# Kernel tuning notes

Measured on AMD Instinct MI355X. Metric: run time of the kernel, lower is better.

The kernel has to match this reference:

```python
import jax, jax.numpy as jnp
import numpy as np

RANK = 16
LN_EPS = 1e-5


def _layer_norm(x, eps=LN_EPS):
    mu = jnp.mean(x, axis=-1, keepdims=True)
    var = jnp.var(x, axis=-1, keepdims=True)
    return (x - mu) / jnp.sqrt(var + eps)


def setup_inputs() -> dict:
    key = jax.random.key(0)
    ks = jax.random.split(key, 8)
    B, S, D, M, R = 32, 4096, 160, 16, RANK
    query = jax.random.normal(ks[0], (B, S, D), dtype=jnp.float32)
    interface = jax.random.normal(ks[1], (B, S, D), dtype=jnp.float32)
    memory = jax.random.normal(ks[2], (B, M, D), dtype=jnp.float32)
    sd = 1.0 / np.sqrt(D)
    sr = 1.0 / np.sqrt(R)
    # torch nn.Linear weights: [out_features, in_features]
    W_read_key = jax.random.uniform(ks[3], (R, D), minval=-sd, maxval=sd, dtype=jnp.float32)
    W_read_value = jax.random.uniform(ks[4], (D, R), minval=-sr, maxval=sr, dtype=jnp.float32)
    W_write_key = jax.random.uniform(ks[5], (R, D), minval=-sd, maxval=sd, dtype=jnp.float32)
    W_write_erase = jax.random.uniform(ks[6], (D, R), minval=-sr, maxval=sr, dtype=jnp.float32)
    W_write_add = jax.random.uniform(ks[7], (D, R), minval=-sr, maxval=sr, dtype=jnp.float32)
    return {
        "query": query,
        "interface": interface,
        "memory": memory,
        "W_read_key": W_read_key,
        "W_read_value": W_read_value,
        "W_write_key": W_write_key,
        "W_write_erase": W_write_erase,
        "W_write_add": W_write_add,
    }


def reference(query, interface, memory, W_read_key, W_read_value,
              W_write_key, W_write_erase, W_write_add):
    R = RANK
    # ---- read ----
    q_proj = jnp.einsum('bsd,rd->bsr', query, W_read_key)          # [B,S,R]
    mem_proj = memory[..., :R]                                      # [B,M,R]
    scores = jnp.einsum('bsr,bmr->bsm', q_proj, mem_proj) / jnp.sqrt(jnp.float32(R))
    attn = jax.nn.softmax(scores, axis=-1)                          # [B,S,M]
    content = jnp.einsum('bsm,bmd->bsd', attn, memory)              # [B,S,D]
    read_out = jnp.einsum('bsr,dr->bsd', content[..., :R], W_read_value)
    # ---- write ----
    i_mean = jnp.mean(interface, axis=1)                            # [B,D]
    i_proj = jnp.einsum('bd,rd->br', i_mean, W_write_key)           # [B,R]
    erase = jax.nn.sigmoid(jnp.einsum('br,dr->bd', i_proj, W_write_erase))[:, None, :]
    add = jnp.einsum('br,dr->bd', i_proj, W_write_add)[:, None, :]
    new_memory = _layer_norm(memory * (1.0 - erase) + add)          # [B,M,D]
    return read_out, new_memory
```

## Files before the change

kernel.cpp:

```cpp
#include <hip/hip_runtime.h>
#include <math.h>

#define NB 32
#define NS 4096
#define ND 160
#define ND4 40
#define NM 16
#define NR 16
#define TPB 64
#define NCB (NS / TPB)

__global__ __launch_bounds__(256, 5) void ulm_read_kernel(
    const float* __restrict__ query,
    const float* __restrict__ iface,
    const float* __restrict__ memory,
    const float* __restrict__ Wrk,
    const float* __restrict__ Wrv,
    float* __restrict__ read_out,
    float* __restrict__ ipart)
{
    __shared__ __align__(16) float sK[NM * ND];
    __shared__ __align__(16) float sV[NM * ND];
    __shared__ float sM16[NM * NR];
    __shared__ float4 sIred[4 * ND4];

    const int t = threadIdx.x;
    const int chunk = blockIdx.x;
    const int b = blockIdx.y;
    const int s0 = chunk * TPB;

    {
        int m = t >> 4, r = t & 15;
        sM16[t] = memory[((size_t)b * NM + m) * ND + r];
    }
    __syncthreads();

    if (t < ND) {
        float wk[NR], wv[NR];
#pragma unroll
        for (int r = 0; r < NR; ++r) wk[r] = Wrk[r * ND + t];
        const float4* wrv4 = reinterpret_cast<const float4*>(Wrv + t * NR);
#pragma unroll
        for (int j = 0; j < 4; ++j) {
            float4 v = wrv4[j];
            wv[j * 4 + 0] = v.x; wv[j * 4 + 1] = v.y;
            wv[j * 4 + 2] = v.z; wv[j * 4 + 3] = v.w;
        }
#pragma unroll
        for (int m = 0; m < NM; ++m) {
            float aK = 0.f, aV = 0.f;
#pragma unroll
            for (int r = 0; r < NR; ++r) {
                float mv = sM16[m * NR + r];
                aK += mv * wk[r];
                aV += mv * wv[r];
            }
            sK[m * ND + t] = aK * 0.25f;
            sV[m * ND + t] = aV;
        }
    }
    __syncthreads();

    const float4* sK4 = reinterpret_cast<const float4*>(sK);
    const float4* sV4 = reinterpret_cast<const float4*>(sV);

    const int l = t & 7;
    const int G = t >> 3;
    const int tok0 = G * 2, tok1 = tok0 + 1;

    const float4* q4 = reinterpret_cast<const float4*>(query + ((size_t)b * NS + s0) * ND);

    float sc0[NM], sc1[NM];
#pragma unroll
    for (int m = 0; m < NM; ++m) { sc0[m] = 0.f; sc1[m] = 0.f; }

#pragma unroll
    for (int k = 0; k < 5; ++k) {
        float4 qa = q4[tok0 * ND4 + l + 8 * k];
        float4 qb = q4[tok1 * ND4 + l + 8 * k];
#pragma unroll
        for (int m = 0; m < NM; ++m) {
            float4 kv = sK4[m * ND4 + l + 8 * k];
            sc0[m] += qa.x * kv.x + qa.y * kv.y + qa.z * kv.z + qa.w * kv.w;
            sc1[m] += qb.x * kv.x + qb.y * kv.y + qb.z * kv.z + qb.w * kv.w;
        }
    }
#pragma unroll
    for (int m = 0; m < NM; ++m) {
        sc0[m] += __shfl_xor(sc0[m], 1);
        sc0[m] += __shfl_xor(sc0[m], 2);
        sc0[m] += __shfl_xor(sc0[m], 4);
        sc1[m] += __shfl_xor(sc1[m], 1);
        sc1[m] += __shfl_xor(sc1[m], 2);
        sc1[m] += __shfl_xor(sc1[m], 4);
    }

    float mx0 = -1e30f, mx1 = -1e30f;
#pragma unroll
    for (int m = 0; m < NM; ++m) { mx0 = fmaxf(mx0, sc0[m]); mx1 = fmaxf(mx1, sc1[m]); }
    float sm0 = 0.f, sm1 = 0.f;
#pragma unroll
    for (int m = 0; m < NM; ++m) {
        sc0[m] = __expf(sc0[m] - mx0); sm0 += sc0[m];
        sc1[m] = __expf(sc1[m] - mx1); sm1 += sc1[m];
    }
    float inv0 = 1.f / sm0, inv1 = 1.f / sm1;
#pragma unroll
    for (int m = 0; m < NM; ++m) { sc0[m] *= inv0; sc1[m] *= inv1; }

    const float4* i4 = reinterpret_cast<const float4*>(iface + ((size_t)b * NS + s0) * ND);
    const int w = t >> 6;
#pragma unroll
    for (int k = 0; k < 5; ++k) {
        float4 va = i4[tok0 * ND4 + l + 8 * k];
        float4 vb = i4[tok1 * ND4 + l + 8 * k];
        float x = va.x + vb.x, y = va.y + vb.y;
        float z = va.z + vb.z, u = va.w + vb.w;
#pragma unroll
        for (int off = 8; off <= 32; off <<= 1) {
            x += __shfl_xor(x, off); y += __shfl_xor(y, off);
            z += __shfl_xor(z, off); u += __shfl_xor(u, off);
        }
        if ((t & 63) < 8) sIred[w * ND4 + k * 8 + l] = make_float4(x, y, z, u);
    }

    float4* out4 = reinterpret_cast<float4*>(read_out + ((size_t)b * NS + s0) * ND);
#pragma unroll
    for (int k = 0; k < 5; ++k) {
        float4 o0 = make_float4(0.f, 0.f, 0.f, 0.f);
        float4 o1 = make_float4(0.f, 0.f, 0.f, 0.f);
#pragma unroll
        for (int m = 0; m < NM; ++m) {
            float4 vv = sV4[m * ND4 + l + 8 * k];
            o0.x += sc0[m] * vv.x; o0.y += sc0[m] * vv.y;
            o0.z += sc0[m] * vv.z; o0.w += sc0[m] * vv.w;
            o1.x += sc1[m] * vv.x; o1.y += sc1[m] * vv.y;
            o1.z += sc1[m] * vv.z; o1.w += sc1[m] * vv.w;
        }
        out4[tok0 * ND4 + l + 8 * k] = o0;
        out4[tok1 * ND4 + l + 8 * k] = o1;
    }

    __syncthreads();
    if (t < ND4) {
        float4 a0 = sIred[t], a1 = sIred[ND4 + t];
        float4 a2 = sIred[2 * ND4 + t], a3 = sIred[3 * ND4 + t];
        float4 tot = make_float4(a0.x + a1.x + a2.x + a3.x,
                                 a0.y + a1.y + a2.y + a3.y,
                                 a0.z + a1.z + a2.z + a3.z,
                                 a0.w + a1.w + a2.w + a3.w);
        reinterpret_cast<float4*>(ipart + ((size_t)(b * NCB + chunk)) * ND)[t] = tot;
    }
}

__global__ __launch_bounds__(256) void ulm_write_kernel(
    const float* __restrict__ memory,
    const float* __restrict__ Wwk,
    const float* __restrict__ Wwe,
    const float* __restrict__ Wwa,
    const float* __restrict__ ipart,
    float* __restrict__ new_mem)
{
    __shared__ float sIm[ND];
    __shared__ float sIp[NR];
    __shared__ float sOmE[ND];
    __shared__ float sAdd[ND];

    const int b = blockIdx.x;
    const int t = threadIdx.x;

    if (t < ND) {
        float acc = 0.f;
        for (int c = 0; c < NCB; ++c)
            acc += ipart[((size_t)(b * NCB + c)) * ND + t];
        sIm[t] = acc * (1.0f / NS);
    }
    __syncthreads();

    if (t < NR) {
        float acc = 0.f;
        for (int d = 0; d < ND; ++d) acc += sIm[d] * Wwk[t * ND + d];
        sIp[t] = acc;
    }
    __syncthreads();

    if (t < ND) {
        float e = 0.f, a = 0.f;
#pragma unroll
        for (int r = 0; r < NR; ++r) {
            float ip = sIp[r];
            e += ip * Wwe[t * NR + r];
            a += ip * Wwa[t * NR + r];
        }
        sOmE[t] = 1.0f - 1.0f / (1.0f + __expf(-e));
        sAdd[t] = a;
    }
    __syncthreads();

    const int wave = t >> 6, lane = t & 63;
    for (int m = wave; m < NM; m += 4) {
        const float* mrow = memory + ((size_t)b * NM + m) * ND;
        float v0 = mrow[lane] * sOmE[lane] + sAdd[lane];
        float v1 = mrow[lane + 64] * sOmE[lane + 64] + sAdd[lane + 64];
        float v2 = 0.f;
        const bool has2 = lane < 32;
        if (has2) v2 = mrow[lane + 128] * sOmE[lane + 128] + sAdd[lane + 128];
        float s  = v0 + v1 + v2;
        float sq = v0 * v0 + v1 * v1 + v2 * v2;
#pragma unroll
        for (int off = 32; off; off >>= 1) {
            s  += __shfl_xor(s, off);
            sq += __shfl_xor(sq, off);
        }
        float mu   = s * (1.0f / ND);
        float var  = sq * (1.0f / ND) - mu * mu;
        float rstd = rsqrtf(var + 1e-5f);
        float* orow = new_mem + ((size_t)b * NM + m) * ND;
        orow[lane]      = (v0 - mu) * rstd;
        orow[lane + 64] = (v1 - mu) * rstd;
        if (has2) orow[lane + 128] = (v2 - mu) * rstd;
    }
}

extern "C" void kernel_launch(void* const* d_in, const int* in_sizes, int n_in,
                              void* d_out, int out_size, void* d_ws, size_t ws_size,
                              hipStream_t stream) {
    const float* query  = (const float*)d_in[0];
    const float* iface  = (const float*)d_in[1];
    const float* memory = (const float*)d_in[2];
    const float* Wrk    = (const float*)d_in[3];
    const float* Wrv    = (const float*)d_in[4];
    const float* Wwk    = (const float*)d_in[5];
    const float* Wwe    = (const float*)d_in[6];
    const float* Wwa    = (const float*)d_in[7];

    float* read_out = (float*)d_out;
    float* new_mem  = (float*)d_out + (size_t)NB * NS * ND;
    float* ipart    = (float*)d_ws;

    dim3 grid1(NCB, NB);
    ulm_read_kernel<<<grid1, 256, 0, stream>>>(query, iface, memory, Wrk, Wrv,
                                               read_out, ipart);
    ulm_write_kernel<<<NB, 256, 0, stream>>>(memory, Wwk, Wwe, Wwa, ipart, new_mem);
}
```

Baseline: 62.71 us.

## Precompute folded K/V per batch in separate kernel and stream output stores

Moves the per-batch fold of memory with the read weights out of every read block into a small pre-kernel that writes the K/V tables to workspace. Read blocks then load K/V straight from global memory (L1/L2-cached) instead of recomputing them into shared memory, and the occupancy hint rises from 5 to 6. Outputs are written with nontemporal stores, and the partial-sum loop in the write kernel is unrolled. The cost is an extra kernel launch, and the inner loops now read K/V from global memory rather than LDS.

```diff
diff --git a/kernel.cpp b/kernel.cpp
--- a/kernel.cpp
+++ b/kernel.cpp
@@ -10,31 +10,22 @@
 #define TPB 64
 #define NCB (NS / TPB)
 
-__global__ __launch_bounds__(256, 5) void ulm_read_kernel(
-    const float* __restrict__ query,
-    const float* __restrict__ iface,
+typedef float f32x4 __attribute__((ext_vector_type(4)));
+
+__global__ __launch_bounds__(256) void ulm_fold_kv(
     const float* __restrict__ memory,
     const float* __restrict__ Wrk,
     const float* __restrict__ Wrv,
-    float* __restrict__ read_out,
-    float* __restrict__ ipart)
+    float* __restrict__ kvbuf)
 {
-    __shared__ __align__(16) float sK[NM * ND];
-    __shared__ __align__(16) float sV[NM * ND];
     __shared__ float sM16[NM * NR];
-    __shared__ float4 sIred[4 * ND4];
-
+    const int b = blockIdx.x;
     const int t = threadIdx.x;
-    const int chunk = blockIdx.x;
-    const int b = blockIdx.y;
-    const int s0 = chunk * TPB;
-
     {
         int m = t >> 4, r = t & 15;
         sM16[t] = memory[((size_t)b * NM + m) * ND + r];
     }
     __syncthreads();
-
     if (t < ND) {
         float wk[NR], wv[NR];
 #pragma unroll
@@ -46,6 +37,7 @@
             wv[j * 4 + 0] = v.x; wv[j * 4 + 1] = v.y;
             wv[j * 4 + 2] = v.z; wv[j * 4 + 3] = v.w;
         }
+        float* kb = kvbuf + (size_t)b * 2 * NM * ND;
 #pragma unroll
         for (int m = 0; m < NM; ++m) {
             float aK = 0.f, aV = 0.f;
@@ -55,14 +47,28 @@
                 aK += mv * wk[r];
                 aV += mv * wv[r];
             }
-            sK[m * ND + t] = aK * 0.25f;
-            sV[m * ND + t] = aV;
-        }
-    }
-    __syncthreads();
-
-    const float4* sK4 = reinterpret_cast<const float4*>(sK);
-    const float4* sV4 = reinterpret_cast<const float4*>(sV);
+            kb[m * ND + t]           = aK * 0.25f;
+            kb[NM * ND + m * ND + t] = aV;
+        }
+    }
+}
+
+__global__ __launch_bounds__(256, 6) void ulm_read_kernel(
+    const float* __restrict__ query,
+    const float* __restrict__ iface,
+    const float* __restrict__ kvbuf,
+    float* __restrict__ read_out,
+    float* __restrict__ ipart)
+{
+    __shared__ float4 sIred[4 * ND4];
+
+    const int t = threadIdx.x;
+    const int chunk = blockIdx.x;
+    const int b = blockIdx.y;
+    const int s0 = chunk * TPB;
+
+    const float4* kK4 = reinterpret_cast<const float4*>(kvbuf + (size_t)b * 2 * NM * ND);
+    const float4* kV4 = kK4 + NM * ND4;
 
     const int l = t & 7;
     const int G = t >> 3;
@@ -80,7 +86,7 @@
         float4 qb = q4[tok1 * ND4 + l + 8 * k];
 #pragma unroll
         for (int m = 0; m < NM; ++m) {
-            float4 kv = sK4[m * ND4 + l + 8 * k];
+            float4 kv = kK4[m * ND4 + l + 8 * k];
             sc0[m] += qa.x * kv.x + qa.y * kv.y + qa.z * kv.z + qa.w * kv.w;
             sc1[m] += qb.x * kv.x + qb.y * kv.y + qb.z * kv.z + qb.w * kv.w;
         }
@@ -131,14 +137,18 @@
         float4 o1 = make_float4(0.f, 0.f, 0.f, 0.f);
 #pragma unroll
         for (int m = 0; m < NM; ++m) {
-            float4 vv = sV4[m * ND4 + l + 8 * k];
+            float4 vv = kV4[m * ND4 + l + 8 * k];
             o0.x += sc0[m] * vv.x; o0.y += sc0[m] * vv.y;
             o0.z += sc0[m] * vv.z; o0.w += sc0[m] * vv.w;
             o1.x += sc1[m] * vv.x; o1.y += sc1[m] * vv.y;
             o1.z += sc1[m] * vv.z; o1.w += sc1[m] * vv.w;
         }
-        out4[tok0 * ND4 + l + 8 * k] = o0;
-        out4[tok1 * ND4 + l + 8 * k] = o1;
+        f32x4 ov0; ov0.x = o0.x; ov0.y = o0.y; ov0.z = o0.z; ov0.w = o0.w;
+        f32x4 ov1; ov1.x = o1.x; ov1.y = o1.y; ov1.z = o1.z; ov1.w = o1.w;
+        __builtin_nontemporal_store(ov0,
+            reinterpret_cast<f32x4*>(out4 + tok0 * ND4 + l + 8 * k));
+        __builtin_nontemporal_store(ov1,
+            reinterpret_cast<f32x4*>(out4 + tok1 * ND4 + l + 8 * k));
     }
 
     __syncthreads();
@@ -171,6 +181,7 @@
 
     if (t < ND) {
         float acc = 0.f;
+#pragma unroll 8
         for (int c = 0; c < NCB; ++c)
             acc += ipart[((size_t)(b * NCB + c)) * ND + t];
         sIm[t] = acc * (1.0f / NS);
@@ -237,9 +248,11 @@
     float* read_out = (float*)d_out;
     float* new_mem  = (float*)d_out + (size_t)NB * NS * ND;
     float* ipart    = (float*)d_ws;
-
+    float* kvbuf    = (float*)d_ws + (size_t)NB * NCB * ND;
+
+    ulm_fold_kv<<<NB, 256, 0, stream>>>(memory, Wrk, Wrv, kvbuf);
     dim3 grid1(NCB, NB);
-    ulm_read_kernel<<<grid1, 256, 0, stream>>>(query, iface, memory, Wrk, Wrv,
+    ulm_read_kernel<<<grid1, 256, 0, stream>>>(query, iface, kvbuf,
                                                read_out, ipart);
     ulm_write_kernel<<<NB, 256, 0, stream>>>(memory, Wwk, Wwe, Wwa, ipart, new_mem);
 }
```

New measurement: 176.1 us. +180.9%, slower.

## Compute attention scores and value projection with bf16 MFMA

Applied to the files above, without the earlier changes.

Rewrites the read kernel so the query-key score product and the attention-value product run on 16x16x32 bf16 MFMA instructions, with operands rounded from fp32 to bf16. Each block now covers 256 tokens, processed by each wave in sets of 16, and the softmax probabilities pass through shared memory to be repacked as MFMA fragments. The interface sum becomes a per-lane accumulation over 8 tokens. This cuts the scalar FMA work of the fp32 kernel, at the cost of bf16 precision in the scores and outputs and fewer blocks in the grid.

```diff
diff --git a/kernel.cpp b/kernel.cpp
--- a/kernel.cpp
+++ b/kernel.cpp
@@ -1,4 +1,5 @@
 #include <hip/hip_runtime.h>
+#include <hip/hip_bf16.h>
 #include <math.h>
 
 #define NB 32
@@ -7,10 +8,29 @@
 #define ND4 40
 #define NM 16
 #define NR 16
-#define TPB 64
+#define TPB 256
 #define NCB (NS / TPB)
 
-__global__ __launch_bounds__(256, 5) void ulm_read_kernel(
+typedef float  f32x4  __attribute__((ext_vector_type(4)));
+typedef short  bf16x8 __attribute__((ext_vector_type(8)));
+typedef unsigned int u32x4 __attribute__((ext_vector_type(4)));
+
+__device__ __forceinline__ unsigned bfpair(float lo, float hi) {
+    union { float f; unsigned u; } a, c;
+    a.f = lo; c.f = hi;
+    unsigned ua = (a.u + 0x7FFFu + ((a.u >> 16) & 1u)) >> 16;
+    unsigned uc = (c.u + 0x7FFFu + ((c.u >> 16) & 1u)) >> 16;
+    return (uc << 16) | (ua & 0xFFFFu);
+}
+
+__device__ __forceinline__ bf16x8 mkfrag(unsigned w0, unsigned w1,
+                                         unsigned w2, unsigned w3) {
+    union { u32x4 u; bf16x8 h; } x;
+    x.u = (u32x4){w0, w1, w2, w3};
+    return x.h;
+}
+
+__global__ __launch_bounds__(256) void ulm_read_kernel(
     const float* __restrict__ query,
     const float* __restrict__ iface,
     const float* __restrict__ memory,
@@ -19,20 +39,21 @@
     float* __restrict__ read_out,
     float* __restrict__ ipart)
 {
-    __shared__ __align__(16) float sK[NM * ND];
-    __shared__ __align__(16) float sV[NM * ND];
+    __shared__ __align__(16) float sKV[2 * NM * ND];
     __shared__ float sM16[NM * NR];
+    __shared__ unsigned sP[4][16 * 10];
     __shared__ float4 sIred[4 * ND4];
 
     const int t = threadIdx.x;
     const int chunk = blockIdx.x;
     const int b = blockIdx.y;
     const int s0 = chunk * TPB;
-
-    {
-        int m = t >> 4, r = t & 15;
-        sM16[t] = memory[((size_t)b * NM + m) * ND + r];
-    }
+    const int w  = t >> 6;
+    const int l  = t & 63;
+    const int lr = l & 15;
+    const int lg = l >> 4;
+
+    sM16[t] = memory[((size_t)b * NM + (t >> 4)) * ND + (t & 15)];
     __syncthreads();
 
     if (t < ND) {
@@ -55,92 +76,118 @@
                 aK += mv * wk[r];
                 aV += mv * wv[r];
             }
-            sK[m * ND + t] = aK * 0.25f;
-            sV[m * ND + t] = aV;
-        }
-    }
-    __syncthreads();
-
-    const float4* sK4 = reinterpret_cast<const float4*>(sK);
-    const float4* sV4 = reinterpret_cast<const float4*>(sV);
-
-    const int l = t & 7;
-    const int G = t >> 3;
-    const int tok0 = G * 2, tok1 = tok0 + 1;
-
-    const float4* q4 = reinterpret_cast<const float4*>(query + ((size_t)b * NS + s0) * ND);
-
-    float sc0[NM], sc1[NM];
-#pragma unroll
-    for (int m = 0; m < NM; ++m) { sc0[m] = 0.f; sc1[m] = 0.f; }
-
+            sKV[m * ND + t]           = aK * 0.25f;
+            sKV[NM * ND + m * ND + t] = aV;
+        }
+    }
+    __syncthreads();
+
+    bf16x8 kf[5];
+#pragma unroll
+    for (int kb = 0; kb < 5; ++kb) {
+        const float* src = &sKV[lr * ND + lg * 8 + kb * 32];
+        float4 a = *reinterpret_cast<const float4*>(src);
+        float4 c = *reinterpret_cast<const float4*>(src + 4);
+        kf[kb] = mkfrag(bfpair(a.x, a.y), bfpair(a.z, a.w),
+                        bfpair(c.x, c.y), bfpair(c.z, c.w));
+    }
+
+    bf16x8 vf[10];
+#pragma unroll
+    for (int d = 0; d < 10; ++d) {
+        if (lg < 2) {
+            float f0 = sKV[NM*ND + (lg*8 + 0) * ND + d*16 + lr];
+            float f1 = sKV[NM*ND + (lg*8 + 1) * ND + d*16 + lr];
+            float f2 = sKV[NM*ND + (lg*8 + 2) * ND + d*16 + lr];
+            float f3 = sKV[NM*ND + (lg*8 + 3) * ND + d*16 + lr];
+            float f4 = sKV[NM*ND + (lg*8 + 4) * ND + d*16 + lr];
+            float f5 = sKV[NM*ND + (lg*8 + 5) * ND + d*16 + lr];
+            float f6 = sKV[NM*ND + (lg*8 + 6) * ND + d*16 + lr];
+            float f7 = sKV[NM*ND + (lg*8 + 7) * ND + d*16 + lr];
+            vf[d] = mkfrag(bfpair(f0, f1), bfpair(f2, f3),
+                           bfpair(f4, f5), bfpair(f6, f7));
+        } else {
+            vf[d] = mkfrag(0u, 0u, 0u, 0u);
+        }
+    }
+
+    const size_t base = (size_t)b * NS * ND;
+    const float4* q4  = reinterpret_cast<const float4*>(query + base) + (size_t)s0 * ND4;
+    float4* out4      = reinterpret_cast<float4*>(read_out + base) + (size_t)s0 * ND4;
+    const int wtok0 = w * 64;
+    unsigned* pl = &sP[w][0];
+
+#pragma unroll 1
+    for (int set = 0; set < 4; ++set) {
+        const int tok = wtok0 + set * 16 + lr;
+
+        float4 qr[10];
+#pragma unroll
+        for (int kb = 0; kb < 5; ++kb) {
+            qr[2*kb]   = q4[(size_t)tok * ND4 + lg * 2 + kb * 8];
+            qr[2*kb+1] = q4[(size_t)tok * ND4 + lg * 2 + kb * 8 + 1];
+        }
+
+        f32x4 D = {0.f, 0.f, 0.f, 0.f};
+#pragma unroll
+        for (int kb = 0; kb < 5; ++kb) {
+            bf16x8 qf = mkfrag(bfpair(qr[2*kb].x,   qr[2*kb].y),
+                               bfpair(qr[2*kb].z,   qr[2*kb].w),
+                               bfpair(qr[2*kb+1].x, qr[2*kb+1].y),
+                               bfpair(qr[2*kb+1].z, qr[2*kb+1].w));
+            D = __builtin_amdgcn_mfma_f32_16x16x32_bf16(kf[kb], qf, D, 0, 0, 0);
+        }
+
+        float mx = fmaxf(fmaxf(D[0], D[1]), fmaxf(D[2], D[3]));
+        mx = fmaxf(mx, __shfl_xor(mx, 16));
+        mx = fmaxf(mx, __shfl_xor(mx, 32));
+        float e0 = __expf(D[0] - mx), e1 = __expf(D[1] - mx);
+        float e2 = __expf(D[2] - mx), e3 = __expf(D[3] - mx);
+        float sm = e0 + e1 + e2 + e3;
+        sm += __shfl_xor(sm, 16);
+        sm += __shfl_xor(sm, 32);
+        float inv = 1.f / sm;
+        e0 *= inv; e1 *= inv; e2 *= inv; e3 *= inv;
+
+        pl[lr * 10 + lg * 2 + 0] = bfpair(e0, e1);
+        pl[lr * 10 + lg * 2 + 1] = bfpair(e2, e3);
+        asm volatile("s_waitcnt lgkmcnt(0)" ::: "memory");
+        int pb = (lg < 2) ? (lr * 10 + lg * 4) : 0;
+        bf16x8 pf = mkfrag(pl[pb], pl[pb + 1], pl[pb + 2], pl[pb + 3]);
+
+#pragma unroll
+        for (int d = 0; d < 10; ++d) {
+            f32x4 D2 = {0.f, 0.f, 0.f, 0.f};
+            D2 = __builtin_amdgcn_mfma_f32_16x16x32_bf16(vf[d], pf, D2, 0, 0, 0);
+            out4[(size_t)tok * ND4 + d * 4 + lg] =
+                make_float4(D2[0], D2[1], D2[2], D2[3]);
+        }
+    }
+
+    const float4* i4 = reinterpret_cast<const float4*>(iface + base) + (size_t)s0 * ND4;
+    const int l8 = l & 7, g8 = l >> 3;
+    float4 ia[5];
+#pragma unroll
+    for (int k = 0; k < 5; ++k) ia[k] = make_float4(0.f, 0.f, 0.f, 0.f);
+#pragma unroll
+    for (int i = 0; i < 8; ++i) {
+        int tk = wtok0 + g8 * 8 + i;
+#pragma unroll
+        for (int k = 0; k < 5; ++k) {
+            float4 v = i4[(size_t)tk * ND4 + l8 + 8 * k];
+            ia[k].x += v.x; ia[k].y += v.y; ia[k].z += v.z; ia[k].w += v.w;
+        }
+    }
 #pragma unroll
     for (int k = 0; k < 5; ++k) {
-        float4 qa = q4[tok0 * ND4 + l + 8 * k];
-        float4 qb = q4[tok1 * ND4 + l + 8 * k];
-#pragma unroll
-        for (int m = 0; m < NM; ++m) {
-            float4 kv = sK4[m * ND4 + l + 8 * k];
-            sc0[m] += qa.x * kv.x + qa.y * kv.y + qa.z * kv.z + qa.w * kv.w;
-            sc1[m] += qb.x * kv.x + qb.y * kv.y + qb.z * kv.z + qb.w * kv.w;
-        }
-    }
-#pragma unroll
-    for (int m = 0; m < NM; ++m) {
-        sc0[m] += __shfl_xor(sc0[m], 1);
-        sc0[m] += __shfl_xor(sc0[m], 2);
-        sc0[m] += __shfl_xor(sc0[m], 4);
-        sc1[m] += __shfl_xor(sc1[m], 1);
-        sc1[m] += __shfl_xor(sc1[m], 2);
-        sc1[m] += __shfl_xor(sc1[m], 4);
-    }
-
-    float mx0 = -1e30f, mx1 = -1e30f;
-#pragma unroll
-    for (int m = 0; m < NM; ++m) { mx0 = fmaxf(mx0, sc0[m]); mx1 = fmaxf(mx1, sc1[m]); }
-    float sm0 = 0.f, sm1 = 0.f;
-#pragma unroll
-    for (int m = 0; m < NM; ++m) {
-        sc0[m] = __expf(sc0[m] - mx0); sm0 += sc0[m];
-        sc1[m] = __expf(sc1[m] - mx1); sm1 += sc1[m];
-    }
-    float inv0 = 1.f / sm0, inv1 = 1.f / sm1;
-#pragma unroll
-    for (int m = 0; m < NM; ++m) { sc0[m] *= inv0; sc1[m] *= inv1; }
-
-    const float4* i4 = reinterpret_cast<const float4*>(iface + ((size_t)b * NS + s0) * ND);
-    const int w = t >> 6;
-#pragma unroll
-    for (int k = 0; k < 5; ++k) {
-        float4 va = i4[tok0 * ND4 + l + 8 * k];
-        float4 vb = i4[tok1 * ND4 + l + 8 * k];
-        float x = va.x + vb.x, y = va.y + vb.y;
-        float z = va.z + vb.z, u = va.w + vb.w;
+        float x = ia[k].x, y = ia[k].y, z = ia[k].z, u = ia[k].w;
 #pragma unroll
         for (int off = 8; off <= 32; off <<= 1) {
             x += __shfl_xor(x, off); y += __shfl_xor(y, off);
             z += __shfl_xor(z, off); u += __shfl_xor(u, off);
         }
-        if ((t & 63) < 8) sIred[w * ND4 + k * 8 + l] = make_float4(x, y, z, u);
-    }
-
-    float4* out4 = reinterpret_cast<float4*>(read_out + ((size_t)b * NS + s0) * ND);
-#pragma unroll
-    for (int k = 0; k < 5; ++k) {
-        float4 o0 = make_float4(0.f, 0.f, 0.f, 0.f);
-        float4 o1 = make_float4(0.f, 0.f, 0.f, 0.f);
-#pragma unroll
-        for (int m = 0; m < NM; ++m) {
-            float4 vv = sV4[m * ND4 + l + 8 * k];
-            o0.x += sc0[m] * vv.x; o0.y += sc0[m] * vv.y;
-            o0.z += sc0[m] * vv.z; o0.w += sc0[m] * vv.w;
-            o1.x += sc1[m] * vv.x; o1.y += sc1[m] * vv.y;
-            o1.z += sc1[m] * vv.z; o1.w += sc1[m] * vv.w;
-        }
-        out4[tok0 * ND4 + l + 8 * k] = o0;
-        out4[tok1 * ND4 + l + 8 * k] = o1;
-    }
-
+        if (l < 8) sIred[w * ND4 + k * 8 + l8] = make_float4(x, y, z, u);
+    }
     __syncthreads();
     if (t < ND4) {
         float4 a0 = sIred[t], a1 = sIred[ND4 + t];
@@ -171,6 +218,7 @@
 
     if (t < ND) {
         float acc = 0.f;
+#pragma unroll
         for (int c = 0; c < NCB; ++c)
             acc += ipart[((size_t)(b * NCB + c)) * ND + t];
         sIm[t] = acc * (1.0f / NS);
```

Result: faster. 56.12 us (-10.5%).
